# Kernel tuning notes

Measured on AMD Instinct MI355X. Metric: run time of the kernel, lower is better.

## Reference

```python
import jax, jax.numpy as jnp
import numpy as np


def _run_lstm(x, W, U, b, mask=None):
    """Keras-style LSTM returning final hidden state.
    x: [N, T, D] float; W: [D, 4u]; U: [u, 4u]; b: [4u]; mask: [N, T] bool or None.
    Gate order i, f, g(c), o as in Keras. Masked steps carry state through.
    """
    N, T, D = x.shape
    units = U.shape[0]
    xt = jnp.transpose(x, (1, 0, 2))  # [T, N, D]
    if mask is not None:
        mt = jnp.transpose(mask, (1, 0))[:, :, None]  # [T, N, 1]
        xs = (xt, mt)
    else:
        xs = xt

    def step(carry, inp):
        h, c = carry
        if mask is not None:
            x_t, m = inp
        else:
            x_t = inp
        z = x_t @ W + h @ U + b  # [N, 4u]
        i, f, g, o = jnp.split(z, 4, axis=-1)
        i = jax.nn.sigmoid(i)
        f = jax.nn.sigmoid(f)
        g = jnp.tanh(g)
        o = jax.nn.sigmoid(o)
        c_new = f * c + i * g
        h_new = o * jnp.tanh(c_new)
        if mask is not None:
            h_new = jnp.where(m, h_new, h)
            c_new = jnp.where(m, c_new, c)
        return (h_new, c_new), None

    h0 = jnp.zeros((N, units), dtype=x.dtype)
    c0 = jnp.zeros((N, units), dtype=x.dtype)
    (hT, _), _ = jax.lax.scan(step, (h0, c0), xs)
    return hT


def setup_inputs() -> dict:
    key = jax.random.key(0)
    ks = jax.random.split(key, 10)
    B, T, S, D = 256, 256, 20, 1
    U1, U2 = 32, 24  # inner / outer LSTM units
    sc = 0.1
    x = jax.random.normal(ks[0], (B, T, S, D), dtype=jnp.float32)
    lengths = jax.random.randint(ks[1], (B,), 1, T + 1, dtype=jnp.int32)
    Wi = jax.random.normal(ks[2], (D, 4 * U1), dtype=jnp.float32) * sc
    Ui = jax.random.normal(ks[3], (U1, 4 * U1), dtype=jnp.float32) * sc
    bi = jnp.zeros((4 * U1,), dtype=jnp.float32)
    Wo = jax.random.normal(ks[4], (U1, 4 * U2), dtype=jnp.float32) * sc
    Uo = jax.random.normal(ks[5], (U2, 4 * U2), dtype=jnp.float32) * sc
    bo = jnp.zeros((4 * U2,), dtype=jnp.float32)
    Wd = jax.random.normal(ks[6], (U2, 1), dtype=jnp.float32) * sc
    bd = jnp.zeros((1,), dtype=jnp.float32)
    return {"x": x, "lengths": lengths, "Wi": Wi, "Ui": Ui, "bi": bi,
            "Wo": Wo, "Uo": Uo, "bo": bo, "Wd": Wd, "bd": bd}


def reference(x, lengths, Wi, Ui, bi, Wo, Uo, bo, Wd, bd):
    B, T, S, D = x.shape
    # TimeDistributed(LSTM(32)): run inner LSTM over each outer step (inference, dropout off)
    rows = x.reshape(B * T, S, D)
    h_inner = _run_lstm(rows, Wi, Ui, bi)          # [B*T, 32]
    feats = h_inner.reshape(B, T, -1)              # [B, T, 32]
    # Outer LSTM(24) with ragged-length mask (Keras mask semantics: carry state)
    mask = jnp.arange(T)[None, :] < lengths[:, None]  # [B, T]
    h_outer = _run_lstm(feats, Wo, Uo, bo, mask)   # [B, 24]
    # Dense sigmoid head
    return jax.nn.sigmoid(h_outer @ Wd + bd)       # [B, 1]
```

## Files before the change

kernel.cpp:

```cpp
#include <hip/hip_runtime.h>

#define B_  256
#define T_  256
#define S_  20
#define U1  32
#define G1  128
#define U2  24
#define G2  96
#define NT  16

typedef __attribute__((ext_vector_type(8))) short short8;
typedef __attribute__((ext_vector_type(4))) float f32x4;

__device__ __forceinline__ float sigmoidf_(float x) {
    return __builtin_amdgcn_rcpf(1.0f + __builtin_amdgcn_exp2f(x * -1.44269504f));
}
__device__ __forceinline__ float tanhf_fast(float x) {
    return 1.0f - 2.0f * __builtin_amdgcn_rcpf(1.0f + __builtin_amdgcn_exp2f(x * 2.88539008f));
}

__device__ __forceinline__ unsigned short f2bf(float a) {
    unsigned int u = __float_as_uint(a);
    u += 0x7FFFu + ((u >> 16) & 1u);
    return (unsigned short)(u >> 16);
}
__device__ __forceinline__ unsigned int pack2bf(float a, float b) {
    unsigned int ua = __float_as_uint(a); ua += 0x7FFFu + ((ua >> 16) & 1u);
    unsigned int ub = __float_as_uint(b); ub += 0x7FFFu + ((ub >> 16) & 1u);
    return (ua >> 16) | (ub & 0xFFFF0000u);
}
union frag_u { short8 v; unsigned int u[4]; };
union h2x  { unsigned int u32; _Float16 h[2]; };

__global__ __attribute__((amdgpu_flat_work_group_size(512, 512)))
__attribute__((amdgpu_waves_per_eu(2, 2)))
void fused_kernel(
    const float* __restrict__ x,
    const int*   __restrict__ lengths,
    const float* __restrict__ Wi,
    const float* __restrict__ Ui,
    const float* __restrict__ bi,
    const float* __restrict__ Wo,
    const float* __restrict__ Uo,
    const float* __restrict__ bo,
    const float* __restrict__ Wd,
    const float* __restrict__ bd,
    float* __restrict__ out)
{
    __shared__ __align__(16) _Float16      Pl[T_][G2];
    __shared__ __align__(16) unsigned short hbb[8][16][40];
    __shared__ unsigned int flags[NT];
    const int b    = blockIdx.x;
    const int len  = lengths[b];
    const int tid  = threadIdx.x;
    const int w    = __builtin_amdgcn_readfirstlane(tid >> 6);
    const int lane = tid & 63;
    const int q    = lane >> 4;
    const int n    = lane & 15;

    if (tid < NT) flags[tid] = 0;
    __syncthreads();

    frag_u Bui[8];
#pragma unroll
    for (int tt = 0; tt < 8; ++tt)
#pragma unroll
        for (int k2 = 0; k2 < 4; ++k2)
            Bui[tt].u[k2] = pack2bf(Ui[(8 * q + 2 * k2) * G1 + 16 * tt + n],
                                    Ui[(8 * q + 2 * k2 + 1) * G1 + 16 * tt + n]);
    frag_u Bwo[6];
#pragma unroll
    for (int tt = 0; tt < 6; ++tt)
#pragma unroll
        for (int k2 = 0; k2 < 4; ++k2)
            Bwo[tt].u[k2] = pack2bf(Wo[(8 * q + 2 * k2) * G2 + 16 * tt + n],
                                    Wo[(8 * q + 2 * k2 + 1) * G2 + 16 * tt + n]);
    float bi_l[8], Wi_l[8], bo_l[6];
#pragma unroll
    for (int tt = 0; tt < 8; ++tt) { bi_l[tt] = bi[16 * tt + n]; Wi_l[tt] = Wi[16 * tt + n]; }
#pragma unroll
    for (int tt = 0; tt < 6; ++tt) bo_l[tt] = bo[16 * tt + n];
    int pcol[6];
#pragma unroll
    for (int tt = 0; tt < 6; ++tt) {
        const int col = 16 * tt + n;
        const int g = col / 24;
        pcol[tt] = (col - 24 * g) * 4 + g;
    }

    int tl[3]; int ntl;
    if (w == 0)      { tl[0] = 0; tl[1] = 0; tl[2] = 0; ntl = 1; }
    else if (w == 1) { tl[0] = 1; tl[1] = 8; tl[2] = 9; ntl = 3; }
    else             { tl[0] = w; tl[1] = w + 8; tl[2] = 0; ntl = 2; }

#pragma unroll 1
    for (int i = 0; i < ntl; ++i) {
        const int tile = tl[i];
        const int wt0  = tile * 16;
        if (wt0 >= len) break;

        const float* xr = x + (size_t)(b * T_ + wt0 + 4 * q) * S_;
        float c[2][4];
#pragma unroll
        for (int uh = 0; uh < 2; ++uh)
#pragma unroll
            for (int r = 0; r < 4; ++r) c[uh][r] = 0.0f;

        float xc[4];
#pragma unroll
        for (int r = 0; r < 4; ++r) xc[r] = xr[r * S_];

        {
            f32x4 acc[8];
#pragma unroll
            for (int tt = 0; tt < 8; ++tt)
#pragma unroll
                for (int r = 0; r < 4; ++r)
                    acc[tt][r] = bi_l[tt] + xc[r] * Wi_l[tt];
#pragma unroll
            for (int uh = 0; uh < 2; ++uh)
#pragma unroll
                for (int r = 0; r < 4; ++r) {
                    const float iv = sigmoidf_(acc[0 + uh][r]);
                    const float fv = sigmoidf_(acc[2 + uh][r]);
                    const float gv = tanhf_fast(acc[4 + uh][r]);
                    const float ov = sigmoidf_(acc[6 + uh][r]);
                    c[uh][r] = fv * c[uh][r] + iv * gv;
                    hbb[w][4 * q + r][n + 16 * uh] = f2bf(ov * tanhf_fast(c[uh][r]));
                }
        }
#pragma unroll
        for (int r = 0; r < 4; ++r) xc[r] = xr[r * S_ + 1];

#pragma unroll 1
        for (int s = 1; s < S_; ++s) {
            const int sn = (s + 1 < S_) ? s + 1 : S_ - 1;
            float xnx[4];
#pragma unroll
            for (int r = 0; r < 4; ++r) xnx[r] = xr[r * S_ + sn];

            f32x4 acc[8];
#pragma unroll
            for (int tt = 0; tt < 8; ++tt)
#pragma unroll
                for (int r = 0; r < 4; ++r)
                    acc[tt][r] = bi_l[tt] + xc[r] * Wi_l[tt];

            const short8 A = *(const short8*)&hbb[w][n][8 * q];
#pragma unroll
            for (int tt = 0; tt < 8; ++tt)
                acc[tt] = __builtin_amdgcn_mfma_f32_16x16x32_bf16(A, Bui[tt].v, acc[tt], 0, 0, 0);

#pragma unroll
            for (int uh = 0; uh < 2; ++uh)
#pragma unroll
                for (int r = 0; r < 4; ++r) {
                    const float iv = sigmoidf_(acc[0 + uh][r]);
                    const float fv = sigmoidf_(acc[2 + uh][r]);
                    const float gv = tanhf_fast(acc[4 + uh][r]);
                    const float ov = sigmoidf_(acc[6 + uh][r]);
                    c[uh][r] = fv * c[uh][r] + iv * gv;
                    hbb[w][4 * q + r][n + 16 * uh] = f2bf(ov * tanhf_fast(c[uh][r]));
                }
#pragma unroll
            for (int r = 0; r < 4; ++r) xc[r] = xnx[r];
        }

        {
            const short8 A = *(const short8*)&hbb[w][n][8 * q];
            f32x4 accp[6];
#pragma unroll
            for (int tt = 0; tt < 6; ++tt) {
#pragma unroll
                for (int r = 0; r < 4; ++r) accp[tt][r] = bo_l[tt];
                accp[tt] = __builtin_amdgcn_mfma_f32_16x16x32_bf16(A, Bwo[tt].v, accp[tt], 0, 0, 0);
            }
#pragma unroll
            for (int r = 0; r < 4; ++r) {
                const int tr = wt0 + 4 * q + r;
#pragma unroll
                for (int tt = 0; tt < 6; ++tt)
                    Pl[tr][pcol[tt]] = (_Float16)accp[tt][r];
            }
        }
        __hip_atomic_store(&flags[tile], 1u, __ATOMIC_RELEASE, __HIP_MEMORY_SCOPE_WORKGROUP);
    }

    if (w != 0) return;

    const int half = lane >> 5;
    const int sub  = lane & 31;
    const int u    = (sub < U2) ? sub : U2 - 1;

    float wA[U2], wB[U2];
#pragma unroll
    for (int k = 0; k < U2; ++k) {
        wA[k] = Uo[k * G2 + (2 * half) * U2 + u];
        wB[k] = Uo[k * G2 + (2 * half + 1) * U2 + u];
    }

    auto ldrow = [&](int t) -> f32x4 {
        const uint2 raw = *reinterpret_cast<const uint2*>(&Pl[t][4 * u]);
        h2x a, c2; a.u32 = raw.x; c2.u32 = raw.y;
        f32x4 r;
        r[0] = (float)a.h[0];  r[1] = (float)a.h[1];
        r[2] = (float)c2.h[0]; r[3] = (float)c2.h[1];
        return r;
    };

    f32x4 cur = ldrow(0);
    float cu, hu;
    {
        const float ig = sigmoidf_(cur[0]);
        const float gg = tanhf_fast(cur[2]);
        const float og = sigmoidf_(cur[3]);
        cu = ig * gg;
        hu = og * tanhf_fast(cu);
    }
    int wtile = 0;
    f32x4 nxt = ldrow((1 < len) ? 1 : 0);

#pragma unroll 1
    for (int t = 1; t < len; ++t) {
        const int tn = (t + 1 < len) ? (t + 1) : (len - 1);
        const int ttile = tn >> 4;
        if (ttile != wtile) {
            while (__hip_atomic_load(&flags[ttile], __ATOMIC_ACQUIRE,
                                     __HIP_MEMORY_SCOPE_WORKGROUP) == 0u)
                __builtin_amdgcn_s_sleep(1);
            wtile = ttile;
        }
        const f32x4 pf = ldrow(tn);

        float hk[U2];
#pragma unroll
        for (int k = 0; k < U2; ++k)
            hk[k] = __int_as_float(__builtin_amdgcn_readlane(__float_as_int(hu), k));

        const float pA = half ? nxt[2] : nxt[0];
        const float pB = half ? nxt[3] : nxt[1];
        float a0 = pA, a1 = 0.0f, a2 = 0.0f, a3 = 0.0f;
        float b0 = pB, b1 = 0.0f, b2 = 0.0f, b3 = 0.0f;
#pragma unroll
        for (int k = 0; k < U2; k += 4) {
            a0 += hk[k]     * wA[k];     b0 += hk[k]     * wB[k];
            a1 += hk[k + 1] * wA[k + 1]; b1 += hk[k + 1] * wB[k + 1];
            a2 += hk[k + 2] * wA[k + 2]; b2 += hk[k + 2] * wB[k + 2];
            a3 += hk[k + 3] * wA[k + 3]; b3 += hk[k + 3] * wB[k + 3];
        }
        const float zA = (a0 + a1) + (a2 + a3);
        const float zB = (b0 + b1) + (b2 + b3);
        const float oA = __shfl_xor(zA, 32);
        const float oB = __shfl_xor(zB, 32);

        const float z_i = half ? oA : zA;
        const float z_f = half ? oB : zB;
        const float z_g = half ? zA : oA;
        const float z_o = half ? zB : oB;

        const float ig = sigmoidf_(z_i);
        const float fg = sigmoidf_(z_f);
        const float gg = tanhf_fast(z_g);
        const float og = sigmoidf_(z_o);
        cu = fg * cu + ig * gg;
        hu = og * tanhf_fast(cu);

        nxt = pf;
    }

    float acc = bd[0];
#pragma unroll
    for (int k = 0; k < U2; ++k)
        acc += __int_as_float(__builtin_amdgcn_readlane(__float_as_int(hu), k)) * Wd[k];
    if (lane == 0) out[b] = sigmoidf_(acc);
}

extern "C" void kernel_launch(void* const* d_in, const int* in_sizes, int n_in,
                              void* d_out, int out_size, void* d_ws, size_t ws_size,
                              hipStream_t stream) {
    const float* x       = (const float*)d_in[0];
    const int*   lengths = (const int*)  d_in[1];
    const float* Wi      = (const float*)d_in[2];
    const float* Ui      = (const float*)d_in[3];
    const float* bi      = (const float*)d_in[4];
    const float* Wo      = (const float*)d_in[5];
    const float* Uo      = (const float*)d_in[6];
    const float* bo      = (const float*)d_in[7];
    const float* Wd      = (const float*)d_in[8];
    const float* bd      = (const float*)d_in[9];
    float* out = (float*)d_out;

    fused_kernel<<<dim3(B_), dim3(512), 0, stream>>>(
        x, lengths, Wi, Ui, bi, Wo, Uo, bo, Wd, bd, out);
}
```

Baseline: 161.7 us.

## Process two sequences per block with dual consumer waves and tile-chunked outer loop

Each block now handles two batch rows. Waves 0 and 4 run the serial outer LSTM recurrences while the other six waves produce inner-LSTM projections for both rows, interleaved three tiles apart. The grid is halved to 128 blocks, so the serial recurrences run concurrently inside a block rather than across separate blocks. The consumer loop is split into 16-step chunks, which removes per-step flag checks, and each lane now loads only its two needed projection values. The risks are fewer producer waves per sequence and a shared-memory footprint that doubles.

```diff
diff --git a/kernel.cpp b/kernel.cpp
--- a/kernel.cpp
+++ b/kernel.cpp
@@ -47,18 +47,16 @@
     const float* __restrict__ bd,
     float* __restrict__ out)
 {
-    __shared__ __align__(16) _Float16      Pl[T_][G2];
+    __shared__ __align__(16) _Float16      Pl[2][T_][G2];
     __shared__ __align__(16) unsigned short hbb[8][16][40];
-    __shared__ unsigned int flags[NT];
-    const int b    = blockIdx.x;
-    const int len  = lengths[b];
+    __shared__ unsigned int flags[2 * NT];
     const int tid  = threadIdx.x;
     const int w    = __builtin_amdgcn_readfirstlane(tid >> 6);
     const int lane = tid & 63;
     const int q    = lane >> 4;
     const int n    = lane & 15;
 
-    if (tid < NT) flags[tid] = 0;
+    if (tid < 2 * NT) flags[tid] = 0;
     __syncthreads();
 
     frag_u Bui[8];
@@ -88,18 +86,23 @@
         pcol[tt] = (col - 24 * g) * 4 + g;
     }
 
-    int tl[3]; int ntl;
-    if (w == 0)      { tl[0] = 0; tl[1] = 0; tl[2] = 0; ntl = 1; }
-    else if (w == 1) { tl[0] = 1; tl[1] = 8; tl[2] = 9; ntl = 3; }
-    else             { tl[0] = w; tl[1] = w + 8; tl[2] = 0; ntl = 2; }
+    int ps, base, ntl;
+    const bool consumer = (w == 0) || (w == 4);
+    if (consumer) { ps = (w == 4); base = 0; ntl = 1; }
+    else {
+        const int p = (w < 4) ? (w - 1) : (w - 2);
+        ps = p & 1; base = 1 + (p >> 1); ntl = 5;
+    }
+    const int bs  = blockIdx.x * 2 + ps;
+    const int len = lengths[bs];
 
 #pragma unroll 1
     for (int i = 0; i < ntl; ++i) {
-        const int tile = tl[i];
+        const int tile = base + 3 * i;
         const int wt0  = tile * 16;
         if (wt0 >= len) break;
 
-        const float* xr = x + (size_t)(b * T_ + wt0 + 4 * q) * S_;
+        const float* xr = x + (size_t)(bs * T_ + wt0 + 4 * q) * S_;
         float c[2][4];
 #pragma unroll
         for (int uh = 0; uh < 2; ++uh)
@@ -180,13 +183,14 @@
                 const int tr = wt0 + 4 * q + r;
 #pragma unroll
                 for (int tt = 0; tt < 6; ++tt)
-                    Pl[tr][pcol[tt]] = (_Float16)accp[tt][r];
+                    Pl[ps][tr][pcol[tt]] = (_Float16)accp[tt][r];
             }
         }
-        __hip_atomic_store(&flags[tile], 1u, __ATOMIC_RELEASE, __HIP_MEMORY_SCOPE_WORKGROUP);
-    }
-
-    if (w != 0) return;
+        __hip_atomic_store(&flags[ps * NT + tile], 1u, __ATOMIC_RELEASE,
+                           __HIP_MEMORY_SCOPE_WORKGROUP);
+    }
+
+    if (!consumer) return;
 
     const int half = lane >> 5;
     const int sub  = lane & 31;
@@ -199,80 +203,114 @@
         wB[k] = Uo[k * G2 + (2 * half + 1) * U2 + u];
     }
 
-    auto ldrow = [&](int t) -> f32x4 {
-        const uint2 raw = *reinterpret_cast<const uint2*>(&Pl[t][4 * u]);
-        h2x a, c2; a.u32 = raw.x; c2.u32 = raw.y;
-        f32x4 r;
-        r[0] = (float)a.h[0];  r[1] = (float)a.h[1];
-        r[2] = (float)c2.h[0]; r[3] = (float)c2.h[1];
-        return r;
+    auto ld2 = [&](int t) -> float2 {
+        h2x pp; pp.u32 = *reinterpret_cast<const unsigned int*>(&Pl[ps][t][4 * u + 2 * half]);
+        return make_float2((float)pp.h[0], (float)pp.h[1]);
     };
 
-    f32x4 cur = ldrow(0);
     float cu, hu;
     {
-        const float ig = sigmoidf_(cur[0]);
-        const float gg = tanhf_fast(cur[2]);
-        const float og = sigmoidf_(cur[3]);
+        const float2 r0 = ld2(0);
+        const float zA = r0.x, zB = r0.y;
+        const float oA = __shfl_xor(zA, 32);
+        const float oB = __shfl_xor(zB, 32);
+        const float z_i = half ? oA : zA;
+        const float z_g = half ? zA : oA;
+        const float z_o = half ? zB : oB;
+        const float ig = sigmoidf_(z_i);
+        const float gg = tanhf_fast(z_g);
+        const float og = sigmoidf_(z_o);
         cu = ig * gg;
         hu = og * tanhf_fast(cu);
     }
-    int wtile = 0;
-    f32x4 nxt = ldrow((1 < len) ? 1 : 0);
+
+    int t = 1, tile = 0;
+    int tend = (16 < len) ? 16 : len;
+    float2 nxt = ld2((1 < len) ? 1 : 0);
 
 #pragma unroll 1
-    for (int t = 1; t < len; ++t) {
-        const int tn = (t + 1 < len) ? (t + 1) : (len - 1);
-        const int ttile = tn >> 4;
-        if (ttile != wtile) {
-            while (__hip_atomic_load(&flags[ttile], __ATOMIC_ACQUIRE,
+    while (t < len) {
+#pragma unroll 1
+        for (; t + 1 < tend; ++t) {
+            const float2 pf = ld2(t + 1);
+
+            float hk[U2];
+#pragma unroll
+            for (int k = 0; k < U2; ++k)
+                hk[k] = __int_as_float(__builtin_amdgcn_readlane(__float_as_int(hu), k));
+
+            float a0 = nxt.x, a1 = 0.0f, b0 = nxt.y, b1 = 0.0f;
+#pragma unroll
+            for (int k = 0; k < U2; k += 2) {
+                a0 += hk[k]     * wA[k];     b0 += hk[k]     * wB[k];
+                a1 += hk[k + 1] * wA[k + 1]; b1 += hk[k + 1] * wB[k + 1];
+            }
+            const float zA = a0 + a1;
+            const float zB = b0 + b1;
+            const float oA = __shfl_xor(zA, 32);
+            const float oB = __shfl_xor(zB, 32);
+
+            const float z_i = half ? oA : zA;
+            const float z_f = half ? oB : zB;
+            const float z_g = half ? zA : oA;
+            const float z_o = half ? zB : oB;
+
+            const float ig = sigmoidf_(z_i);
+            const float fg = sigmoidf_(z_f);
+            const float gg = tanhf_fast(z_g);
+            const float og = sigmoidf_(z_o);
+            cu = fg * cu + ig * gg;
+            hu = og * tanhf_fast(cu);
+            nxt = pf;
+        }
+
+        float2 pf = nxt;
+        if (tend < len) {
+            ++tile;
+            while (__hip_atomic_load(&flags[ps * NT + tile], __ATOMIC_ACQUIRE,
                                      __HIP_MEMORY_SCOPE_WORKGROUP) == 0u)
                 __builtin_amdgcn_s_sleep(1);
-            wtile = ttile;
-        }
-        const f32x4 pf = ldrow(tn);
-
-        float hk[U2];
-#pragma unroll
-        for (int k = 0; k < U2; ++k)
-            hk[k] = __int_as_float(__builtin_amdgcn_readlane(__float_as_int(hu), k));
-
-        const float pA = half ? nxt[2] : nxt[0];
-        const float pB = half ? nxt[3] : nxt[1];
-        float a0 = pA, a1 = 0.0f, a2 = 0.0f, a3 = 0.0f;
-        float b0 = pB, b1 = 0.0f, b2 = 0.0f, b3 = 0.0f;
-#pragma unroll
-        for (int k = 0; k < U2; k += 4) {
-            a0 += hk[k]     * wA[k];     b0 += hk[k]     * wB[k];
-            a1 += hk[k + 1] * wA[k + 1]; b1 += hk[k + 1] * wB[k + 1];
-            a2 += hk[k + 2] * wA[k + 2]; b2 += hk[k + 2] * wB[k + 2];
-            a3 += hk[k + 3] * wA[k + 3]; b3 += hk[k + 3] * wB[k + 3];
-        }
-        const float zA = (a0 + a1) + (a2 + a3);
-        const float zB = (b0 + b1) + (b2 + b3);
-        const float oA = __shfl_xor(zA, 32);
-        const float oB = __shfl_xor(zB, 32);
-
-        const float z_i = half ? oA : zA;
-        const float z_f = half ? oB : zB;
-        const float z_g = half ? zA : oA;
-        const float z_o = half ? zB : oB;
-
-        const float ig = sigmoidf_(z_i);
-        const float fg = sigmoidf_(z_f);
-        const float gg = tanhf_fast(z_g);
-        const float og = sigmoidf_(z_o);
-        cu = fg * cu + ig * gg;
-        hu = og * tanhf_fast(cu);
-
+            pf = ld2(tend);
+        }
+        {
+            float hk[U2];
+#pragma unroll
+            for (int k = 0; k < U2; ++k)
+                hk[k] = __int_as_float(__builtin_amdgcn_readlane(__float_as_int(hu), k));
+
+            float a0 = nxt.x, a1 = 0.0f, b0 = nxt.y, b1 = 0.0f;
+#pragma unroll
+            for (int k = 0; k < U2; k += 2) {
+                a0 += hk[k]     * wA[k];     b0 += hk[k]     * wB[k];
+                a1 += hk[k + 1] * wA[k + 1]; b1 += hk[k + 1] * wB[k + 1];
+            }
+            const float zA = a0 + a1;
+            const float zB = b0 + b1;
+            const float oA = __shfl_xor(zA, 32);
+            const float oB = __shfl_xor(zB, 32);
+
+            const float z_i = half ? oA : zA;
+            const float z_f = half ? oB : zB;
+            const float z_g = half ? zA : oA;
+            const float z_o = half ? zB : oB;
+
+            const float ig = sigmoidf_(z_i);
+            const float fg = sigmoidf_(z_f);
+            const float gg = tanhf_fast(z_g);
+            const float og = sigmoidf_(z_o);
+            cu = fg * cu + ig * gg;
+            hu = og * tanhf_fast(cu);
+        }
+        ++t;
         nxt = pf;
+        tend = (tend + 16 < len) ? tend + 16 : len;
     }
 
     float acc = bd[0];
 #pragma unroll
     for (int k = 0; k < U2; ++k)
         acc += __int_as_float(__builtin_amdgcn_readlane(__float_as_int(hu), k)) * Wd[k];
-    if (lane == 0) out[b] = sigmoidf_(acc);
+    if (lane == 0) out[bs] = sigmoidf_(acc);
 }
 
 extern "C" void kernel_launch(void* const* d_in, const int* in_sizes, int n_in,
@@ -290,6 +328,6 @@
     const float* bd      = (const float*)d_in[9];
     float* out = (float*)d_out;
 
-    fused_kernel<<<dim3(B_), dim3(512), 0, stream>>>(
+    fused_kernel<<<dim3(B_ / 2), dim3(512), 0, stream>>>(
         x, lengths, Wi, Ui, bi, Wo, Uo, bo, Wd, bd, out);
 }
```

Result: slower. 213.2 us (+31.9%).
